# Kernel tuning notes

Measured on AMD Instinct MI355X. Metric: run time of the kernel, lower is better.

The kernel has to match this reference:

```python
import jax, jax.numpy as jnp
import numpy as np

H = 16      # num_heads
D = 64      # hidden_size per head
IN = 1024   # input_size = H*D
B, S = 4, 2048

def setup_inputs() -> dict:
    key = jax.random.key(0)
    ks = jax.random.split(key, 5)
    scale = 1.0 / np.sqrt(IN)
    return {
        "x": jax.random.normal(ks[0], (B, S, IN), dtype=jnp.float32),
        "Wq": jax.random.normal(ks[1], (IN, H * D), dtype=jnp.float32) * scale,
        "bq": jnp.zeros((H * D,), dtype=jnp.float32),
        "Wk": jax.random.normal(ks[2], (IN, H * D), dtype=jnp.float32) * scale,
        "bk": jnp.zeros((H * D,), dtype=jnp.float32),
        "Wv": jax.random.normal(ks[3], (IN, H * D), dtype=jnp.float32) * scale,
        "bv": jnp.zeros((H * D,), dtype=jnp.float32),
        "Wo": jax.random.normal(ks[4], (H * D, IN), dtype=jnp.float32) * scale,
        "bo": jnp.zeros((IN,), dtype=jnp.float32),
    }

def reference(x, Wq, bq, Wk, bk, Wv, bv, Wo, bo):
    b, s, _ = x.shape
    # projections -> [b, h, s, d]
    def split_heads(t):
        return t.reshape(b, s, H, D).transpose(0, 2, 1, 3)
    q = split_heads(x @ Wq + bq)
    k = split_heads(x @ Wk + bk)
    v = split_heads(x @ Wv + bv)
    scores = jnp.einsum('bhqd,bhkd->bhqk', q, k) / jnp.sqrt(jnp.float32(D))
    probs = jax.nn.softmax(scores, axis=-1)            # [b,h,s,s]
    attn = jnp.einsum('bhqk,bhkd->bhqd', probs, v)     # [b,h,s,d]
    attn = attn.transpose(0, 2, 1, 3).reshape(b, s, H * D)
    out = attn @ Wo + bo
    return out, jnp.mean(probs, axis=1)
```

## Files before the change

kernel.cpp:

```cpp
#include <hip/hip_runtime.h>

typedef __attribute__((ext_vector_type(8))) short s8v;
typedef __attribute__((ext_vector_type(4))) short s4v;
typedef __attribute__((ext_vector_type(4))) float f4v;

#define DEV __device__ __forceinline__

DEV short b16(float f) {
  unsigned u = __builtin_bit_cast(unsigned, f);
  u = (u + 0x7fffu + ((u >> 16) & 1u)) >> 16;
  return (short)u;
}

DEV unsigned pk2(float a, float b) {
#if __has_builtin(__builtin_amdgcn_cvt_pk_bf16_f32)
  auto p = __builtin_amdgcn_cvt_pk_bf16_f32(a, b);
  return __builtin_bit_cast(unsigned, p);
#else
  return (unsigned)(unsigned short)b16(a) | ((unsigned)(unsigned short)b16(b) << 16);
#endif
}

DEV float fexp2(float x) {
#if __has_builtin(__builtin_amdgcn_exp2f)
  return __builtin_amdgcn_exp2f(x);
#else
  return exp2f(x);
#endif
}

DEV void gl_lds16(const short* g, short* l) {
  __builtin_amdgcn_global_load_lds((const __attribute__((address_space(1))) void*)g,
                                   (__attribute__((address_space(3))) void*)l, 16, 0, 0);
}

#define WAIT_VM(N) asm volatile("s_waitcnt vmcnt(" #N ")" ::: "memory")
#define WAIT_LGKM0() asm volatile("s_waitcnt lgkmcnt(0)" ::: "memory")
#define BAR() __builtin_amdgcn_s_barrier()

__global__ __launch_bounds__(256) void prep(const float* __restrict__ x, short* __restrict__ xb,
                                            const float* __restrict__ W0, const float* __restrict__ W1,
                                            const float* __restrict__ W2, const float* __restrict__ W3,
                                            short* __restrict__ Wt) {
  const int tid = threadIdx.x;
  if (blockIdx.x < 8192) {
    int i = blockIdx.x * 256 + tid;
    float4 v = ((const float4*)x)[i];
    s4v o; o.x = b16(v.x); o.y = b16(v.y); o.z = b16(v.z); o.w = b16(v.w);
    ((s4v*)xb)[i] = o;
  } else {
    int wid = blockIdx.x - 8192;
    const int mat = wid >> 9;
    const float* W = mat == 0 ? W0 : (mat == 1 ? W1 : (mat == 2 ? W2 : W3));
    short* out = Wt + (long)mat * 1048576;
    int id = (wid & 511) * 256 + tid;
    int k8 = id >> 10;
    int n  = id & 1023;
    s8v o;
#pragma unroll
    for (int j = 0; j < 8; ++j) o[j] = b16(W[(k8 * 8 + j) * 1024 + n]);
    *(s8v*)&out[n * 1024 + k8 * 8] = o;
  }
}

__global__ __launch_bounds__(256) void gemm_qkv(const short* __restrict__ A,
                                                const short* __restrict__ Wt,
                                                const float* __restrict__ bq,
                                                const float* __restrict__ bk,
                                                const float* __restrict__ bv,
                                                short* __restrict__ Cb,
                                                short* __restrict__ Vt, float qscale) {
  __shared__ short AB[32768];
  int n = blockIdx.x + 24 * blockIdx.y;
  int id = (n & 7) * 192 + (n >> 3);
  const int nx = id % 24, my = id / 24;
  const int mat = nx >> 3;
  const short* Bt = Wt + (long)mat * 1048576;
  const float* bias = mat == 0 ? bq : (mat == 1 ? bk : bv);
  short* Cout = Cb + (long)mat * 8388608;
  const float scale = mat == 0 ? qscale : 1.0f;
  const int m0 = my * 128, n0 = (nx & 7) * 128;
  const int tid = threadIdx.x;
  const int w = tid >> 6, lane = tid & 63, quad = lane >> 4, l15 = lane & 15;
  const int wm = w >> 1, wn = w & 1;
  const int lr = lane >> 3, lc = (lane & 7) * 8;
  f4v acc[4][4] = {};
#pragma unroll
  for (int i = 0; i < 4; ++i) {
    int c = i * 4 + w;
    int r = c * 8 + lr;
    gl_lds16(&A[(m0 + r) * 1024 + lc], &AB[c * 512]);
    gl_lds16(&Bt[(n0 + r) * 1024 + lc], &AB[8192 + c * 512]);
  }
  for (int t = 0; t < 16; ++t) {
    const int cur = (t & 1) * 16384;
    WAIT_VM(0);
    WAIT_LGKM0();
    BAR();
    if (t < 15) {
      const int nxt = ((t + 1) & 1) * 16384;
      const int k0 = (t + 1) * 64;
#pragma unroll
      for (int i = 0; i < 4; ++i) {
        int c = i * 4 + w;
        int r = c * 8 + lr;
        gl_lds16(&A[(m0 + r) * 1024 + k0 + lc], &AB[nxt + c * 512]);
        gl_lds16(&Bt[(n0 + r) * 1024 + k0 + lc], &AB[nxt + 8192 + c * 512]);
      }
    }
    const short* As = &AB[cur];
    const short* Bs = &AB[cur + 8192];
#pragma unroll
    for (int kk = 0; kk < 2; ++kk) {
      s8v af[4], bf[4];
#pragma unroll
      for (int mt = 0; mt < 4; ++mt) af[mt] = *(const s8v*)&As[(wm * 64 + mt * 16 + l15) * 64 + kk * 32 + quad * 8];
#pragma unroll
      for (int nt = 0; nt < 4; ++nt) bf[nt] = *(const s8v*)&Bs[(wn * 64 + nt * 16 + l15) * 64 + kk * 32 + quad * 8];
#pragma unroll
      for (int mt = 0; mt < 4; ++mt)
#pragma unroll
        for (int nt = 0; nt < 4; ++nt)
          acc[mt][nt] = __builtin_amdgcn_mfma_f32_16x16x32_bf16(af[mt], bf[nt], acc[mt][nt], 0, 0, 0);
    }
  }
  if (mat == 2) {
    __syncthreads();
    short* T = AB;
#pragma unroll
    for (int nt = 0; nt < 4; ++nt) {
      const int c = wn * 64 + nt * 16 + l15;
      const float bcol = bias[n0 + c];
#pragma unroll
      for (int mt = 0; mt < 4; ++mt) {
        const int sr = wm * 64 + mt * 16 + quad * 4;
#pragma unroll
        for (int r = 0; r < 4; ++r) {
          int s = sr + r;
          T[c * 128 + ((((s >> 3) ^ (c & 15))) << 3) + (s & 7)] = b16(acc[mt][nt][r] + bcol);
        }
      }
    }
    __syncthreads();
    const int b = m0 >> 11, s0 = m0 & 2047, h0 = n0 >> 6;
#pragma unroll
    for (int i = 0; i < 8; ++i) {
      int unit = tid + i * 256;
      int c = unit >> 4, s8 = unit & 15;
      s8v v = *(const s8v*)&T[c * 128 + ((s8 ^ (c & 15)) << 3)];
      *(s8v*)&Vt[(((long)(b * 16 + h0 + (c >> 6)) * 64) + (c & 63)) * 2048 + s0 + s8 * 8] = v;
    }
  } else {
#pragma unroll
    for (int nt = 0; nt < 4; ++nt) {
      const int col = n0 + wn * 64 + nt * 16 + l15;
      const float bcol = bias[col];
#pragma unroll
      for (int mt = 0; mt < 4; ++mt)
#pragma unroll
        for (int r = 0; r < 4; ++r) {
          const int row = m0 + wm * 64 + mt * 16 + quad * 4 + r;
          Cout[row * 1024 + col] = b16((acc[mt][nt][r] + bcol) * scale);
        }
    }
  }
}

__global__ __launch_bounds__(256, 3) void attn_ctx(const short* __restrict__ Q, const short* __restrict__ K,
                                                   const short* __restrict__ Vt,
                                                   float* __restrict__ rbuf, short* __restrict__ ctx) {
  __shared__ __align__(16) char smem[49152];
  short* Ks = (short*)smem;
  short* Vs = (short*)(smem + 16384);
  short* Ps = (short*)(smem + 32768);
  short* Qs = Ps;
  int nlin = blockIdx.x + 32 * (blockIdx.y + 16 * blockIdx.z);
  int bid = (nlin & 7) * 256 + (nlin >> 3);
  const int q64 = bid & 31, h = (bid >> 5) & 15, b = bid >> 9;
  const int tid = threadIdx.x, w = tid >> 6, lane = tid & 63, quad = lane >> 4, l15 = lane & 15;
  const int bh = b * 16 + h, q0 = q64 * 64;

#pragma unroll
  for (int i = 0; i < 2; ++i) {
    int c = tid + i * 256;
    int r = c >> 3, cc = c & 7;
    *(s8v*)&Qs[r * 64 + (((cc ^ (r & 7))) << 3)] =
        *(const s8v*)&Q[((b * 2048 + q0 + r) * 16 + h) * 64 + cc * 8];
  }
  __syncthreads();
  s8v qf[4][2];
#pragma unroll
  for (int nt = 0; nt < 4; ++nt) {
    int r = nt * 16 + l15;
    qf[nt][0] = *(const s8v*)&Qs[r * 64 + ((quad ^ (r & 7)) << 3)];
    qf[nt][1] = *(const s8v*)&Qs[r * 64 + (((4 + quad) ^ (r & 7)) << 3)];
  }
  const short* kbase = &K[((long)(b * 2048) * 16 + h) * 64];
  const short* vbase = &Vt[(long)(bh * 64) * 2048];
  const int krow = w * 8 + (lane >> 3);
  const short* ksrc = kbase + krow * 1024 + (((lane & 7) ^ (lane >> 3)) << 3);
  const int vrow = w * 4 + (lane >> 4);
  const short* vsrc = vbase + vrow * 2048 + (((lane & 15) ^ vrow) << 3);
  f4v o[4] = {};
  f4v lf = {};
  s8v ones;
#pragma unroll
  for (int j = 0; j < 8; ++j) ones[j] = (short)0x3F80;

#pragma unroll
  for (int i = 0; i < 4; ++i) gl_lds16(ksrc + i * 32768, &Ks[(i * 4 + w) * 512]);
#pragma unroll
  for (int i = 0; i < 4; ++i) gl_lds16(vsrc + i * 32768, &Vs[(i * 4 + w) * 512]);
  WAIT_LGKM0();

  for (int kt = 0; kt < 16; ++kt) {
    WAIT_VM(4);
    BAR();
#pragma unroll
    for (int mt = 0; mt < 2; ++mt) {
      int kr = w * 32 + mt * 16 + l15;
      s8v a0 = *(const s8v*)&Ks[kr * 64 + ((quad ^ (kr & 7)) << 3)];
      s8v a1 = *(const s8v*)&Ks[kr * 64 + (((4 + quad) ^ (kr & 7)) << 3)];
#pragma unroll
      for (int nt = 0; nt < 4; ++nt) {
        f4v st = {};
        st = __builtin_amdgcn_mfma_f32_16x16x32_bf16(a0, qf[nt][0], st, 0, 0, 0);
        st = __builtin_amdgcn_mfma_f32_16x16x32_bf16(a1, qf[nt][1], st, 0, 0, 0);
        float e0 = fexp2(st[0]), e1 = fexp2(st[1]);
        float e2 = fexp2(st[2]), e3 = fexp2(st[3]);
        uint2 pp; pp.x = pk2(e0, e1); pp.y = pk2(e2, e3);
        int q = nt * 16 + l15;
        int chunk = (w * 4 + mt * 2 + (quad >> 1)) ^ l15;
        *(uint2*)&Ps[q * 128 + (chunk << 3) + (quad & 1) * 4] = pp;
      }
    }
    WAIT_LGKM0();
    BAR();
    if (kt < 15) {
#pragma unroll
      for (int i = 0; i < 4; ++i) gl_lds16(ksrc + (kt + 1) * 131072 + i * 32768, &Ks[(i * 4 + w) * 512]);
      WAIT_VM(4);
    } else {
      WAIT_VM(0);
    }
    BAR();
#pragma unroll
    for (int kk = 0; kk < 4; ++kk) {
      int qr = w * 16 + l15;
      s8v a = *(const s8v*)&Ps[qr * 128 + (((kk * 4 + quad) ^ (qr & 15)) << 3)];
#pragma unroll
      for (int dt = 0; dt < 4; ++dt) {
        int d = dt * 16 + l15;
        s8v vb = *(const s8v*)&Vs[d * 128 + (((kk * 4 + quad) ^ (d & 15)) << 3)];
        o[dt] = __builtin_amdgcn_mfma_f32_16x16x32_bf16(a, vb, o[dt], 0, 0, 0);
      }
      lf = __builtin_amdgcn_mfma_f32_16x16x32_bf16(a, ones, lf, 0, 0, 0);
    }
    WAIT_LGKM0();
    BAR();
    if (kt < 15) {
#pragma unroll
      for (int i = 0; i < 4; ++i) gl_lds16(vsrc + (kt + 1) * 128 + i * 32768, &Vs[(i * 4 + w) * 512]);
    }
  }

  float rv[4];
#pragma unroll
  for (int r = 0; r < 4; ++r) rv[r] = 1.0f / lf[r];
  if (l15 == 0) {
    f4v t; t[0] = rv[0]; t[1] = rv[1]; t[2] = rv[2]; t[3] = rv[3];
    *(f4v*)&rbuf[bh * 2048 + q0 + w * 16 + quad * 4] = t;
  }
#pragma unroll
  for (int dt = 0; dt < 4; ++dt)
#pragma unroll
    for (int r = 0; r < 4; ++r) {
      int sq = q0 + w * 16 + quad * 4 + r;
      ctx[((b * 2048 + sq) * 16 + h) * 64 + dt * 16 + l15] = b16(o[dt][r] * rv[r]);
    }
}

__global__ __launch_bounds__(256) void tail_fused(const short* __restrict__ A,
                                                  const short* __restrict__ Bt,
                                                  const float* __restrict__ bias,
                                                  float* __restrict__ Cout,
                                                  const short* __restrict__ Q,
                                                  const short* __restrict__ K,
                                                  const float* __restrict__ rbuf,
                                                  float* __restrict__ outm) {
  __shared__ __align__(16) char smem[73728];
  const int tid = threadIdx.x;
  const int w = tid >> 6, lane = tid & 63, quad = lane >> 4, l15 = lane & 15;
  if (blockIdx.x < 512) {
    short* AB = (short*)smem;
    int n = blockIdx.x;
    int id = (n & 7) * 64 + (n >> 3);
    const int m0 = (id >> 3) * 128, n0 = (id & 7) * 128;
    const int wm = w >> 1, wn = w & 1;
    const int lr = lane >> 3, lc = (lane & 7) * 8;
    f4v acc[4][4] = {};
#pragma unroll
    for (int i = 0; i < 4; ++i) {
      int c = i * 4 + w;
      int r = c * 8 + lr;
      gl_lds16(&A[(m0 + r) * 1024 + lc], &AB[c * 512]);
      gl_lds16(&Bt[(n0 + r) * 1024 + lc], &AB[8192 + c * 512]);
    }
    for (int t = 0; t < 16; ++t) {
      const int cur = (t & 1) * 16384;
      WAIT_VM(0);
      WAIT_LGKM0();
      BAR();
      if (t < 15) {
        const int nxt = ((t + 1) & 1) * 16384;
        const int k0 = (t + 1) * 64;
#pragma unroll
        for (int i = 0; i < 4; ++i) {
          int c = i * 4 + w;
          int r = c * 8 + lr;
          gl_lds16(&A[(m0 + r) * 1024 + k0 + lc], &AB[nxt + c * 512]);
          gl_lds16(&Bt[(n0 + r) * 1024 + k0 + lc], &AB[nxt + 8192 + c * 512]);
        }
      }
      const short* As = &AB[cur];
      const short* Bs = &AB[cur + 8192];
#pragma unroll
      for (int kk = 0; kk < 2; ++kk) {
        s8v af[4], bf[4];
#pragma unroll
        for (int mt = 0; mt < 4; ++mt) af[mt] = *(const s8v*)&As[(wm * 64 + mt * 16 + l15) * 64 + kk * 32 + quad * 8];
#pragma unroll
        for (int nt = 0; nt < 4; ++nt) bf[nt] = *(const s8v*)&Bs[(wn * 64 + nt * 16 + l15) * 64 + kk * 32 + quad * 8];
#pragma unroll
        for (int mt = 0; mt < 4; ++mt)
#pragma unroll
          for (int nt = 0; nt < 4; ++nt)
            acc[mt][nt] = __builtin_amdgcn_mfma_f32_16x16x32_bf16(af[mt], bf[nt], acc[mt][nt], 0, 0, 0);
      }
    }
#pragma unroll
    for (int nt = 0; nt < 4; ++nt) {
      const int col = n0 + wn * 64 + nt * 16 + l15;
      const float bcol = bias[col];
#pragma unroll
      for (int mt = 0; mt < 4; ++mt)
#pragma unroll
        for (int r = 0; r < 4; ++r) {
          const int row = m0 + wm * 64 + mt * 16 + quad * 4 + r;
          Cout[row * 1024 + col] = acc[mt][nt][r] + bcol;
        }
    }
  } else {
    short* QsB = (short*)smem;
    short* KsB = (short*)(smem + 32768);
    float* r_all = (float*)(smem + 65536);
    int nlin = blockIdx.x - 512;
    int bid = (nlin & 7) * 128 + (nlin >> 3);
    const int k128 = bid & 15, q128 = (bid >> 4) & 15, b = bid >> 8;
    f4v mn[2][8] = {};
    const int mrow = w * 8 + (lane >> 3);
    const int mck8 = ((lane & 7) ^ (lane >> 3)) << 3;
    const short* qsrc = Q + ((long)(b * 2048 + q128 * 128 + mrow) * 16) * 64 + mck8;
    const short* ksrc = K + ((long)(b * 2048 + k128 * 128 + mrow) * 16) * 64 + mck8;
    const float* rb = rbuf + (long)(b * 16) * 2048 + q128 * 128;
#pragma unroll
    for (int i = 0; i < 2; ++i) {
      int hh = i * 8 + w * 2 + (lane >> 5);
      gl_lds16((const short*)(rb + hh * 2048 + (lane & 31) * 4), (short*)r_all + (i * 4 + w) * 512);
    }
#pragma unroll
    for (int i = 0; i < 4; ++i) gl_lds16(qsrc + i * 32768, QsB + (i * 4 + w) * 512);
#pragma unroll
    for (int i = 0; i < 4; ++i) gl_lds16(ksrc + i * 32768, KsB + (i * 4 + w) * 512);

    for (int h = 0; h < 16; ++h) {
      const int cur = h & 1;
      const short* Qsc = QsB + cur * 8192;
      const short* Ksc = KsB + cur * 8192;
      WAIT_VM(0);
      BAR();
      if (h < 15) {
        short* Qsn = QsB + (cur ^ 1) * 8192;
        short* Ksn = KsB + (cur ^ 1) * 8192;
#pragma unroll
        for (int i = 0; i < 4; ++i) gl_lds16(qsrc + (h + 1) * 64 + i * 32768, Qsn + (i * 4 + w) * 512);
#pragma unroll
        for (int i = 0; i < 4; ++i) gl_lds16(ksrc + (h + 1) * 64 + i * 32768, Ksn + (i * 4 + w) * 512);
      }
      s8v aq[2][2];
#pragma unroll
      for (int qt = 0; qt < 2; ++qt) {
        int r = w * 32 + qt * 16 + l15;
        aq[qt][0] = *(const s8v*)&Qsc[r * 64 + ((quad ^ (r & 7)) << 3)];
        aq[qt][1] = *(const s8v*)&Qsc[r * 64 + (((4 + quad) ^ (r & 7)) << 3)];
      }
      float rr[2][4];
#pragma unroll
      for (int qt = 0; qt < 2; ++qt)
#pragma unroll
        for (int r = 0; r < 4; ++r) rr[qt][r] = r_all[h * 128 + w * 32 + qt * 16 + quad * 4 + r];
#pragma unroll
      for (int ktile = 0; ktile < 8; ++ktile) {
        int kr = ktile * 16 + l15;
        s8v b0 = *(const s8v*)&Ksc[kr * 64 + ((quad ^ (kr & 7)) << 3)];
        s8v b1 = *(const s8v*)&Ksc[kr * 64 + (((4 + quad) ^ (kr & 7)) << 3)];
#pragma unroll
        for (int qt = 0; qt < 2; ++qt) {
          f4v sc = {};
          sc = __builtin_amdgcn_mfma_f32_16x16x32_bf16(aq[qt][0], b0, sc, 0, 0, 0);
          sc = __builtin_amdgcn_mfma_f32_16x16x32_bf16(aq[qt][1], b1, sc, 0, 0, 0);
#pragma unroll
          for (int r = 0; r < 4; ++r)
            mn[qt][ktile][r] += fexp2(sc[r]) * rr[qt][r];
        }
      }
    }
#pragma unroll
    for (int qt = 0; qt < 2; ++qt)
#pragma unroll
      for (int ktile = 0; ktile < 8; ++ktile)
#pragma unroll
        for (int r = 0; r < 4; ++r) {
          long qrow = q128 * 128 + w * 32 + qt * 16 + quad * 4 + r;
          outm[((long)b * 2048 + qrow) * 2048 + k128 * 128 + ktile * 16 + l15] = mn[qt][ktile][r] * 0.0625f;
        }
  }
}

extern "C" void kernel_launch(void* const* d_in, const int* in_sizes, int n_in,
                              void* d_out, int out_size, void* d_ws, size_t ws_size,
                              hipStream_t stream) {
  (void)in_sizes; (void)n_in; (void)out_size; (void)ws_size;
  const float* x  = (const float*)d_in[0];
  const float* Wq = (const float*)d_in[1];
  const float* bq = (const float*)d_in[2];
  const float* Wk = (const float*)d_in[3];
  const float* bk = (const float*)d_in[4];
  const float* Wv = (const float*)d_in[5];
  const float* bv = (const float*)d_in[6];
  const float* Wo = (const float*)d_in[7];
  const float* bo = (const float*)d_in[8];
  float* out  = (float*)d_out;
  float* outm = out + 8388608;

  char* ws = (char*)d_ws;
  short* xb  = (short*)(ws);
  short* Wqt = (short*)(ws + 16777216);
  short* Wot = (short*)(ws + 23068672);
  short* Qb  = (short*)(ws + 25165824);
  short* Kb  = (short*)(ws + 41943040);
  short* Vt  = (short*)(ws + 75497472);
  float* rbuf = (float*)(ws + 58720256);
  short* ctx = xb;

  const float C2 = 0.18033688011112042f;

  prep<<<10240, 256, 0, stream>>>(x, xb, Wq, Wk, Wv, Wo, Wqt);
  gemm_qkv<<<dim3(24, 64), 256, 0, stream>>>(xb, Wqt, bq, bk, bv, Qb, Vt, C2);
  attn_ctx<<<dim3(32, 16, 4), 256, 0, stream>>>(Qb, Kb, Vt, rbuf, ctx);
  tail_fused<<<1536, 256, 0, stream>>>(ctx, Wot, bo, out, Qb, Kb, rbuf, outm);
}
```

Measured before the change: 384.7 us.

## Use three-stage LDS pipeline with K=32 tiles in QKV GEMM

The QKV projection GEMM moves from a double-buffered pipeline with 64-wide K tiles to a triple-buffered ring of 32-wide K tiles, prefetching two stages ahead and waiting with a partial vmcnt. LDS drops from 64KB to 48KB, and launch bounds now request 3 blocks per CU, so more blocks can be resident and hide memory latency. The cost is twice as many barriers per K sweep and tighter register limits, which could cause spills.

```diff
diff --git a/kernel.cpp b/kernel.cpp
--- a/kernel.cpp
+++ b/kernel.cpp
@@ -63,14 +63,14 @@
   }
 }
 
-__global__ __launch_bounds__(256) void gemm_qkv(const short* __restrict__ A,
-                                                const short* __restrict__ Wt,
-                                                const float* __restrict__ bq,
-                                                const float* __restrict__ bk,
-                                                const float* __restrict__ bv,
-                                                short* __restrict__ Cb,
-                                                short* __restrict__ Vt, float qscale) {
-  __shared__ short AB[32768];
+__global__ __launch_bounds__(256, 3) void gemm_qkv(const short* __restrict__ A,
+                                                   const short* __restrict__ Wt,
+                                                   const float* __restrict__ bq,
+                                                   const float* __restrict__ bk,
+                                                   const float* __restrict__ bv,
+                                                   short* __restrict__ Cb,
+                                                   short* __restrict__ Vt, float qscale) {
+  __shared__ short AB[24576];
   int n = blockIdx.x + 24 * blockIdx.y;
   int id = (n & 7) * 192 + (n >> 3);
   const int nx = id % 24, my = id / 24;
@@ -83,46 +83,49 @@
   const int tid = threadIdx.x;
   const int w = tid >> 6, lane = tid & 63, quad = lane >> 4, l15 = lane & 15;
   const int wm = w >> 1, wn = w & 1;
-  const int lr = lane >> 3, lc = (lane & 7) * 8;
+  const int lrA = lane >> 2, lcA = (lane & 3) * 8;
   f4v acc[4][4] = {};
 #pragma unroll
-  for (int i = 0; i < 4; ++i) {
-    int c = i * 4 + w;
-    int r = c * 8 + lr;
-    gl_lds16(&A[(m0 + r) * 1024 + lc], &AB[c * 512]);
-    gl_lds16(&Bt[(n0 + r) * 1024 + lc], &AB[8192 + c * 512]);
-  }
-  for (int t = 0; t < 16; ++t) {
-    const int cur = (t & 1) * 16384;
-    WAIT_VM(0);
+  for (int t0 = 0; t0 < 2; ++t0) {
+    short* Ab = AB + t0 * 8192;
+    const int k0 = t0 * 32;
+#pragma unroll
+    for (int i = 0; i < 2; ++i) {
+      int rb = (i * 4 + w) * 16;
+      gl_lds16(&A[(m0 + rb + lrA) * 1024 + k0 + lcA], Ab + (i * 4 + w) * 512);
+      gl_lds16(&Bt[(n0 + rb + lrA) * 1024 + k0 + lcA], Ab + 4096 + (i * 4 + w) * 512);
+    }
+  }
+  int cb = 0;
+  for (int t = 0; t < 32; ++t) {
+    short* Ab = AB + cb * 8192;
+    if (t < 30) { WAIT_VM(4); } else { WAIT_VM(0); }
     WAIT_LGKM0();
     BAR();
-    if (t < 15) {
-      const int nxt = ((t + 1) & 1) * 16384;
-      const int k0 = (t + 1) * 64;
-#pragma unroll
-      for (int i = 0; i < 4; ++i) {
-        int c = i * 4 + w;
-        int r = c * 8 + lr;
-        gl_lds16(&A[(m0 + r) * 1024 + k0 + lc], &AB[nxt + c * 512]);
-        gl_lds16(&Bt[(n0 + r) * 1024 + k0 + lc], &AB[nxt + 8192 + c * 512]);
-      }
-    }
-    const short* As = &AB[cur];
-    const short* Bs = &AB[cur + 8192];
-#pragma unroll
-    for (int kk = 0; kk < 2; ++kk) {
-      s8v af[4], bf[4];
-#pragma unroll
-      for (int mt = 0; mt < 4; ++mt) af[mt] = *(const s8v*)&As[(wm * 64 + mt * 16 + l15) * 64 + kk * 32 + quad * 8];
-#pragma unroll
-      for (int nt = 0; nt < 4; ++nt) bf[nt] = *(const s8v*)&Bs[(wn * 64 + nt * 16 + l15) * 64 + kk * 32 + quad * 8];
-#pragma unroll
-      for (int mt = 0; mt < 4; ++mt)
-#pragma unroll
-        for (int nt = 0; nt < 4; ++nt)
-          acc[mt][nt] = __builtin_amdgcn_mfma_f32_16x16x32_bf16(af[mt], bf[nt], acc[mt][nt], 0, 0, 0);
-    }
+    if (t < 30) {
+      const int nb = cb >= 1 ? cb - 1 : 2;
+      short* An = AB + nb * 8192;
+      const int k0 = (t + 2) * 32;
+#pragma unroll
+      for (int i = 0; i < 2; ++i) {
+        int rb = (i * 4 + w) * 16;
+        gl_lds16(&A[(m0 + rb + lrA) * 1024 + k0 + lcA], An + (i * 4 + w) * 512);
+        gl_lds16(&Bt[(n0 + rb + lrA) * 1024 + k0 + lcA], An + 4096 + (i * 4 + w) * 512);
+      }
+    }
+    const short* As = Ab;
+    const short* Bs = Ab + 4096;
+    s8v af[4], bf[4];
+#pragma unroll
+    for (int mt = 0; mt < 4; ++mt) af[mt] = *(const s8v*)&As[(wm * 64 + mt * 16 + l15) * 32 + quad * 8];
+#pragma unroll
+    for (int nt = 0; nt < 4; ++nt) bf[nt] = *(const s8v*)&Bs[(wn * 64 + nt * 16 + l15) * 32 + quad * 8];
+#pragma unroll
+    for (int mt = 0; mt < 4; ++mt)
+#pragma unroll
+      for (int nt = 0; nt < 4; ++nt)
+        acc[mt][nt] = __builtin_amdgcn_mfma_f32_16x16x32_bf16(af[mt], bf[nt], acc[mt][nt], 0, 0, 0);
+    cb = cb == 2 ? 0 : cb + 1;
   }
   if (mat == 2) {
     __syncthreads();
```

After: 372.4 us. 1.03x faster.
